# Kernel tuning notes

Hardware: AMD Instinct MI355X
Metric: run time of the kernel (lower is better)

Reference implementation:

```python
import jax, jax.numpy as jnp
import numpy as np

N, E, R, D = 50000, 640000, 200, 128  # nodes, edges, relations, feat dim (in_feat==out_feat)
EPS = 1e-5  # LayerNorm eps
NEG_SLOPE = 0.01  # F.leaky_relu default

def _xavier(k, shape):
    gain = np.sqrt(2.0)  # calculate_gain('relu')
    std = gain * np.sqrt(2.0 / (shape[0] + shape[1]))
    a = np.sqrt(3.0) * std
    return jax.random.uniform(k, shape, jnp.float32, -a, a)

def setup_inputs() -> dict:
    key = jax.random.key(0)
    ks = jax.random.split(key, 10)
    return {
        "node": jax.random.normal(ks[0], (N, D), jnp.float32),
        "rel": jax.random.normal(ks[1], (R, D), jnp.float32),
        "norm": jax.random.uniform(ks[2], (N, 1), jnp.float32),
        "w_triplet": _xavier(ks[3], (3 * D, D)),
        "w_quad": _xavier(ks[4], (D, D)),
        "loop_weight": _xavier(ks[5], (D, D)),
        "evolve_loop_weight": _xavier(ks[6], (D, D)),
        "src": jax.random.randint(ks[7], (E,), 0, N),
        "dst": jax.random.randint(ks[8], (E,), 0, N),
        "etype": jax.random.randint(ks[9], (E,), 0, R),
    }

def reference(node, rel, norm, w_triplet, w_quad, loop_weight, evolve_loop_weight, src, dst, etype):
    # triplet = cat([h_src, rel_emb, h_dst], 1) @ w_triplet, computed blockwise
    # to avoid materializing the [E, 3D] concat.
    W_s, W_r, W_d = w_triplet[:D], w_triplet[D:2 * D], w_triplet[2 * D:]
    triplet = node[src] @ W_s + rel[etype] @ W_r + node[dst] @ W_d  # [E, D]
    # 'fre' not in edata -> sro_fre is zeros; a_triplet = triplet @ w_quad
    a = jax.nn.leaky_relu(triplet @ w_quad, negative_slope=NEG_SLOPE)  # [E, D]
    # edge_softmax: softmax over incoming edges per destination node, per feature
    a_max = jax.ops.segment_max(a, dst, num_segments=N)
    a_max = jnp.where(jnp.isfinite(a_max), a_max, 0.0)  # empty segments -> -inf
    ex = jnp.exp(a - a_max[dst])
    denom = jax.ops.segment_sum(ex, dst, num_segments=N)
    att = ex / denom[dst]
    # weighted scatter-sum aggregation, then apply_func: h * norm
    h = jax.ops.segment_sum(att * triplet, dst, num_segments=N) * norm  # [N, D]
    # self-loop: evolve_loop_weight for in-degree-0 nodes, loop_weight otherwise
    indeg = jax.ops.segment_sum(jnp.ones((E,), jnp.float32), dst, num_segments=N)
    loop = jnp.where((indeg > 0)[:, None], node @ loop_weight, node @ evolve_loop_weight)
    out = h + loop
    # LayerNorm(elementwise_affine=False)
    mu = jnp.mean(out, axis=-1, keepdims=True)
    var = jnp.var(out, axis=-1, keepdims=True)
    return (out - mu) * jax.lax.rsqrt(var + EPS)
```

## Files before the change

### kernel.cpp

```cpp
#include <hip/hip_runtime.h>
#include <hip/hip_bf16.h>

#define D 128
#define LOG2E 1.4426950408889634f

typedef __attribute__((ext_vector_type(8))) short bf16x8;
typedef __attribute__((ext_vector_type(4))) float f32x4;

__device__ __forceinline__ unsigned short f2bf_bits(float f) {
    union { __hip_bfloat16 h; unsigned short u; } c;
    c.h = __float2bfloat16(f);
    return c.u;
}
__device__ __forceinline__ float bfbits2f(unsigned short u) {
    return __uint_as_float(((unsigned)u) << 16);
}
__device__ __forceinline__ float ldf(const void* p, size_t i, int f32) {
    return f32 ? ((const float*)p)[i] : bfbits2f(((const unsigned short*)p)[i]);
}
__device__ __forceinline__ void unpk(unsigned u, float& a, float& b) {
    a = __uint_as_float(u << 16);
    b = __uint_as_float(u & 0xFFFF0000u);
}

__global__ __launch_bounds__(256) void prep_kernel(
    const void* __restrict__ node, const void* __restrict__ wtrip,
    const void* __restrict__ wquad, const void* __restrict__ loopW,
    const void* __restrict__ evoW, unsigned short* __restrict__ wT,
    int* __restrict__ cnt, int* __restrict__ rank,
    const int* __restrict__ dst, int* __restrict__ flag, int E) {
    __shared__ int sflag;
    int tid = threadIdx.x;
    int bad = 0;
    if (tid < 64) {
        for (int j = 0; j < 4; j++) {
            float v = bfbits2f(((const unsigned short*)node)[tid + 64 * j]);
            if (!(fabsf(v) < 1e4f)) bad = 1;
        }
    }
    unsigned long long m = __ballot(bad);
    if (tid == 0) sflag = (m != 0ull) ? 1 : 0;
    __syncthreads();
    int f32 = sflag;
    int bx = blockIdx.x;
    if (bx == 0 && tid == 0) *flag = f32;

    if (bx < 192) {
        int unit = bx * 2 + (tid >> 7);
        int k = unit & 127, mjob = unit >> 7;
        int t = tid & 127;
        float acc = 0.f;
        for (int j = 0; j < D; j++)
            acc += ldf(wtrip, (size_t)mjob * D * D + (size_t)k * D + j, f32) *
                   ldf(wquad, (size_t)j * D + t, f32);
        const int jmap0 = (mjob == 0) ? 0 : (mjob == 1 ? 6 : 2);
        wT[(size_t)jmap0 * D * D + (size_t)t * D + k] = f2bf_bits(acc);
    } else if (bx < 272) {
        int u = bx - 192;
        int jr = u >> 4, seg = u & 15;
        const void* srcp; size_t base; int j;
        switch (jr) {
            case 0: srcp = wtrip; base = 0;             j = 1; break;
            case 1: srcp = wtrip; base = 2 * D * D;     j = 3; break;
            case 2: srcp = loopW; base = 0;             j = 4; break;
            case 3: srcp = evoW;  base = 0;             j = 5; break;
            default: srcp = wtrip; base = (size_t)D * D; j = 7; break;
        }
        for (int c = tid; c < 1024; c += 256) {
            int idx = seg * 1024 + c;
            int n = idx >> 7, k = idx & 127;
            unsigned short b = f32 ? f2bf_bits(((const float*)srcp)[base + (size_t)k * D + n])
                                   : ((const unsigned short*)srcp)[base + (size_t)k * D + n];
            wT[(size_t)j * D * D + (size_t)n * D + k] = b;
        }
    } else {
        int e = (bx - 272) * 256 + tid;
        if (e < E) rank[e] = atomicAdd(&cnt[dst[e]], 1);
    }
}

__global__ void scan_block(const int* __restrict__ cnt, int* __restrict__ offs,
                           int* __restrict__ part, int N) {
    __shared__ int sh[256];
    int tid = threadIdx.x;
    int i = blockIdx.x * 256 + tid;
    int v = (i < N) ? cnt[i] : 0;
    sh[tid] = v;
    __syncthreads();
    for (int o = 1; o < 256; o <<= 1) {
        int t = (tid >= o) ? sh[tid - o] : 0;
        __syncthreads();
        sh[tid] += t;
        __syncthreads();
    }
    if (i < N) offs[i] = sh[tid] - v;
    if (tid == 255) part[blockIdx.x] = sh[255];
}

__global__ void scan_fix(int* __restrict__ offs, const int* __restrict__ part,
                         int N, int E) {
    __shared__ int sh[256];
    int tid = threadIdx.x, b = blockIdx.x;
    sh[tid] = (tid < b) ? part[tid] : 0;
    __syncthreads();
    for (int o = 128; o; o >>= 1) {
        if (tid < o) sh[tid] += sh[tid + o];
        __syncthreads();
    }
    int carry = sh[0];
    int i = b * 256 + tid;
    if (i < N) offs[i] += carry;
    if (b == 0 && tid == 0) offs[N] = E;
}

__global__ __launch_bounds__(512) void gemm_kernel(
    const void* __restrict__ node, const void* __restrict__ rel,
    const unsigned short* __restrict__ wT, const int* __restrict__ cnt,
    unsigned* __restrict__ nodeST, unsigned* __restrict__ nodeDT,
    unsigned* __restrict__ relRT, unsigned* __restrict__ loopSel,
    const int* __restrict__ flag, int N, int R, int nodeBlocks,
    const int* __restrict__ src, const int* __restrict__ dst,
    const int* __restrict__ et, const int* __restrict__ offs,
    const int* __restrict__ rank, unsigned* __restrict__ ePack, int E) {
    __shared__ __align__(16) unsigned short Wt[D][D + 8];

    int bx = blockIdx.x, by = blockIdx.y;
    int tid = threadIdx.y * 64 + threadIdx.x;
    int isRel = 0, jp;
    if (bx >= nodeBlocks) {
        if (by == 1) {
            int e = (bx - nodeBlocks) * 512 + tid;
            if (e < E) {
                int d = dst[e];
                ePack[offs[d] + rank[e]] = (unsigned)src[e] | ((unsigned)et[e] << 20);
            }
            return;
        }
        if (by != 0 || bx - nodeBlocks >= (R + 127) / 128) return;
        isRel = 1;
        jp = 3;
    } else {
        jp = by;
    }

    int f32 = *flag;
    int rows = isRel ? R : N;
    int row0 = (isRel ? bx - nodeBlocks : bx) * 128;
    const void* A = isRel ? rel : node;

    int lane = threadIdx.x, wv = threadIdx.y;
    int l16 = lane & 15, quad = lane >> 4;
    int ar = row0 + wv * 16 + l16;
    int ar_c = ar < rows ? ar : rows - 1;

    int qIdx, tIdx;
    unsigned* O = nullptr;
    switch (jp) {
        case 0: qIdx = 0; tIdx = 1; O = nodeST; break;
        case 1: qIdx = 2; tIdx = 3; O = nodeDT; break;
        case 2: qIdx = 4; tIdx = 5; break;
        default: qIdx = 6; tIdx = 7; O = relRT; break;
    }

    bf16x8 af[4];
#pragma unroll
    for (int kk = 0; kk < 4; kk++) {
        int k = kk * 32 + quad * 8;
        if (f32) {
            const float* Af = (const float*)A + (size_t)ar_c * D + k;
#pragma unroll
            for (int j = 0; j < 8; j++) af[kk][j] = (short)f2bf_bits(Af[j]);
        } else {
            af[kk] = *(const bf16x8*)((const unsigned short*)A + (size_t)ar_c * D + k);
        }
    }

    const unsigned short* gQ = wT + (size_t)qIdx * D * D;
    const unsigned short* gT = wT + (size_t)tIdx * D * D;

    bf16x8 wreg[4], wreg2[4];
#pragma unroll
    for (int i = 0; i < 4; i++) {
        int c = tid + i * 512;
        wreg[i] = *(const bf16x8*)(gQ + (c >> 4) * 128 + (c & 15) * 8);
    }

    f32x4 accQ[8], accT[8];
#pragma unroll
    for (int i = 0; i < 8; i++) {
        accQ[i] = (f32x4){0.f, 0.f, 0.f, 0.f};
        accT[i] = (f32x4){0.f, 0.f, 0.f, 0.f};
    }

    for (int pass = 0; pass < 2; pass++) {
#pragma unroll
        for (int i = 0; i < 4; i++) {
            int c = tid + i * 512;
            *(bf16x8*)(&Wt[c >> 4][(c & 15) * 8]) = wreg[i];
        }
        if (pass == 0) {
#pragma unroll
            for (int i = 0; i < 4; i++) {
                int c = tid + i * 512;
                wreg2[i] = *(const bf16x8*)(gT + (c >> 4) * 128 + (c & 15) * 8);
            }
        }
        __syncthreads();
        f32x4* acc = pass ? accT : accQ;
#pragma unroll
        for (int kk = 0; kk < 4; kk++) {
#pragma unroll
            for (int nt = 0; nt < 8; nt++) {
                bf16x8 bfr = *(const bf16x8*)(&Wt[nt * 16 + l16][kk * 32 + quad * 8]);
                acc[nt] = __builtin_amdgcn_mfma_f32_16x16x32_bf16(af[kk], bfr, acc[nt], 0, 0, 0);
            }
        }
        __syncthreads();
#pragma unroll
        for (int i = 0; i < 4; i++) wreg[i] = wreg2[i];
    }

    int cr0 = row0 + wv * 16 + quad * 4;
    int odd = l16 & 1;
    if (jp != 2) {
#pragma unroll
        for (int r = 0; r < 4; r++) {
            int cr = cr0 + r;
#pragma unroll
            for (int nt = 0; nt < 8; nt++) {
                float vQ = accQ[nt][r] * LOG2E;
                float vT = accT[nt][r];
                float oQ = __shfl_xor(vQ, 1);
                float oT = __shfl_xor(vT, 1);
                unsigned w;
                if (!odd) w = (unsigned)f2bf_bits(vQ) | ((unsigned)f2bf_bits(oQ) << 16);
                else      w = (unsigned)f2bf_bits(oT) | ((unsigned)f2bf_bits(vT) << 16);
                if (cr < rows) O[(size_t)cr * 128 + nt * 16 + l16] = w;
            }
        }
    } else {
#pragma unroll
        for (int r = 0; r < 4; r++) {
            int cr = cr0 + r;
            int deg = (cr < rows) ? cnt[cr] : 0;
#pragma unroll
            for (int nt = 0; nt < 8; nt++) {
                float vL = accQ[nt][r], vE = accT[nt][r];
                float oL = __shfl_xor(vL, 1);
                float oE = __shfl_xor(vE, 1);
                unsigned wl, we;
                if (!odd) {
                    wl = (unsigned)f2bf_bits(vL) | ((unsigned)f2bf_bits(oL) << 16);
                    we = (unsigned)f2bf_bits(vE) | ((unsigned)f2bf_bits(oE) << 16);
                } else {
                    wl = (unsigned)f2bf_bits(oL) | ((unsigned)f2bf_bits(vL) << 16);
                    we = (unsigned)f2bf_bits(oE) | ((unsigned)f2bf_bits(vE) << 16);
                }
                if (cr < rows && !odd)
                    loopSel[(size_t)cr * 64 + nt * 8 + (l16 >> 1)] = (deg > 0) ? wl : we;
            }
        }
    }
}

__global__ __launch_bounds__(256) void agg_kernel(
    const int* __restrict__ offs, const unsigned* __restrict__ ePack,
    const uint2* __restrict__ ST, const uint2* __restrict__ RT,
    const uint2* __restrict__ DT, const unsigned* __restrict__ loopSel,
    const void* __restrict__ normv, void* __restrict__ out,
    const int* __restrict__ flag, int N) {
    int n = blockIdx.x * 4 + threadIdx.y;
    if (n >= N) return;
    int f32 = *flag;
    int lane = threadIdx.x;
    int start = offs[n], end = offs[n + 1];
    int deg = end - start;

    unsigned ul = loopSel[(size_t)n * 64 + lane];
    uint2 ud = DT[(size_t)n * 64 + lane];
    float qd0, qd1, td0, td1, acc0, acc1;
    unpk(ud.x, qd0, qd1);
    unpk(ud.y, td0, td1);
    unpk(ul, acc0, acc1);

    float den0 = 0.f, den1 = 0.f, h0 = 0.f, h1 = 0.f;
#define GATH(PK, US, UR)                                              \
    uint2 US = ST[(size_t)((PK) & 0xFFFFFu) * 64 + lane];             \
    uint2 UR = RT[(size_t)((PK) >> 20) * 64 + lane];
#define EMATH(US, UR)                                                 \
    {                                                                 \
        float qs0, qs1, qr0, qr1, ts0, ts1, tr0, tr1;                 \
        unpk(US.x, qs0, qs1); unpk(UR.x, qr0, qr1);                   \
        unpk(US.y, ts0, ts1); unpk(UR.y, tr0, tr1);                   \
        float q0 = qs0 + qr0 + qd0, q1 = qs1 + qr1 + qd1;             \
        float a0 = q0 > 0.f ? q0 : 0.01f * q0;                        \
        float a1 = q1 > 0.f ? q1 : 0.01f * q1;                        \
        float ex0 = exp2f(a0), ex1 = exp2f(a1);                       \
        den0 += ex0; den1 += ex1;                                     \
        h0 += ex0 * (ts0 + tr0 + td0);                                \
        h1 += ex1 * (ts1 + tr1 + td1);                                \
    }
    int e = start;
    for (; e + 3 < end; e += 4) {
        unsigned p0 = ePack[e], p1 = ePack[e + 1], p2 = ePack[e + 2], p3 = ePack[e + 3];
        GATH(p0, sA, rA)
        GATH(p1, sB, rB)
        GATH(p2, sC, rC)
        GATH(p3, sD, rD)
        EMATH(sA, rA)
        EMATH(sB, rB)
        EMATH(sC, rC)
        EMATH(sD, rD)
    }
    for (; e < end; e++) {
        unsigned pp = ePack[e];
        GATH(pp, sE, rE)
        EMATH(sE, rE)
    }

    float x0, x1;
    if (deg > 0) {
        float nrm = ldf(normv, n, f32);
        x0 = h0 / den0 * nrm + acc0;
        x1 = h1 / den1 * nrm + acc1;
    } else {
        x0 = acc0;
        x1 = acc1;
    }

    float s = x0 + x1, ss = x0 * x0 + x1 * x1;
#pragma unroll
    for (int o = 32; o; o >>= 1) {
        s += __shfl_xor(s, o);
        ss += __shfl_xor(ss, o);
    }
    float mu = s * (1.f / 128.f);
    float var = ss * (1.f / 128.f) - mu * mu;
    float rstd = rsqrtf(var + 1e-5f);
    float y0 = (x0 - mu) * rstd, y1 = (x1 - mu) * rstd;

    if (f32) {
        ((float2*)out)[(size_t)n * 64 + lane] = make_float2(y0, y1);
    } else {
        unsigned ob = (unsigned)f2bf_bits(y0) | ((unsigned)f2bf_bits(y1) << 16);
        ((unsigned*)out)[(size_t)n * 64 + lane] = ob;
    }
}

extern "C" void kernel_launch(void* const* d_in, const int* in_sizes, int n_in,
                              void* d_out, int out_size, void* d_ws, size_t ws_size,
                              hipStream_t stream) {
    const void* node = d_in[0];
    const void* rel = d_in[1];
    const void* normv = d_in[2];
    const void* wtrip = d_in[3];
    const void* wquad = d_in[4];
    const void* loopW = d_in[5];
    const void* evoW = d_in[6];
    const int* src = (const int*)d_in[7];
    const int* dst = (const int*)d_in[8];
    const int* et = (const int*)d_in[9];

    int N = in_sizes[0] / D;
    int R = in_sizes[1] / D;
    int E = in_sizes[7];
    int nb = (N + 255) / 256;
    int nodeBlocks = (N + 127) / 128;
    int relBlocks = (R + 127) / 128;
    int scatBlocks = (E + 511) / 512;

    char* p = (char*)d_ws;
    auto alloc = [&](size_t bytes) -> void* {
        void* r = (void*)p;
        p += (bytes + 255) & ~(size_t)255;
        return r;
    };
    unsigned* nodeST = (unsigned*)alloc((size_t)N * 128 * 4);
    unsigned* nodeDT = (unsigned*)alloc((size_t)N * 128 * 4);
    unsigned* relRT = (unsigned*)alloc((size_t)R * 128 * 4);
    unsigned* loopSel = (unsigned*)alloc((size_t)N * 64 * 4);
    unsigned short* wT = (unsigned short*)alloc((size_t)8 * D * D * 2);
    int* cnt = (int*)alloc((size_t)N * 4);
    int* offs = (int*)alloc((size_t)(N + 1) * 4);
    int* part = (int*)alloc((size_t)(nb + 1) * 4);
    int* rank = (int*)alloc((size_t)E * 4);
    unsigned* ePack = (unsigned*)alloc((size_t)E * 4);
    int* flag = (int*)alloc(4);

    hipMemsetAsync(cnt, 0, (size_t)N * 4, stream);
    prep_kernel<<<272 + (E + 255) / 256, 256, 0, stream>>>(
        node, wtrip, wquad, loopW, evoW, wT, cnt, rank, dst, flag, E);
    scan_block<<<nb, 256, 0, stream>>>(cnt, offs, part, N);
    scan_fix<<<nb, 256, 0, stream>>>(offs, part, N, E);
    int xext = nodeBlocks + (scatBlocks > relBlocks ? scatBlocks : relBlocks);
    gemm_kernel<<<dim3(xext, 3), dim3(64, 8), 0, stream>>>(
        node, rel, wT, cnt, nodeST, nodeDT, relRT, loopSel, flag, N, R, nodeBlocks,
        src, dst, et, offs, rank, ePack, E);
    agg_kernel<<<(N + 3) / 4, dim3(64, 4), 0, stream>>>(
        offs, ePack, (const uint2*)nodeST, (const uint2*)relRT, (const uint2*)nodeDT,
        loopSel, normv, d_out, flag, N);
}
```

Before: 235.2 us.

## Split wavefront into half-waves processing two edges at once with 16-byte gathers

The aggregation kernel now splits each 64-lane wavefront into two 32-lane halves. Each half handles a different edge, and each lane gathers 16 bytes (4 features of q and t) instead of 8. Partial softmax denominators and weighted sums are combined with a cross-half shuffle, the LayerNorm reduction runs over 32 lanes, and only the first half writes the output. The intent is to widen memory transactions and improve parallelism for low-degree nodes, at the cost of an extra shuffle and masked tail handling for odd degrees.

Result: no change. 236.9 us (+0.7%).

```diff
diff --git a/kernel.cpp b/kernel.cpp
--- a/kernel.cpp
+++ b/kernel.cpp
@@ -6,6 +6,9 @@
 
 typedef __attribute__((ext_vector_type(8))) short bf16x8;
 typedef __attribute__((ext_vector_type(4))) float f32x4;
+typedef __attribute__((ext_vector_type(2))) float f32x2;
+typedef __attribute__((ext_vector_type(2))) unsigned u32x2;
+typedef __attribute__((ext_vector_type(4))) unsigned u32x4;
 
 __device__ __forceinline__ unsigned short f2bf_bits(float f) {
     union { __hip_bfloat16 h; unsigned short u; } c;
@@ -18,9 +21,17 @@
 __device__ __forceinline__ float ldf(const void* p, size_t i, int f32) {
     return f32 ? ((const float*)p)[i] : bfbits2f(((const unsigned short*)p)[i]);
 }
-__device__ __forceinline__ void unpk(unsigned u, float& a, float& b) {
-    a = __uint_as_float(u << 16);
-    b = __uint_as_float(u & 0xFFFF0000u);
+__device__ __forceinline__ f32x2 unpk2(unsigned u) {
+    f32x2 r;
+    r.x = __uint_as_float(u << 16);
+    r.y = __uint_as_float(u & 0xFFFF0000u);
+    return r;
+}
+__device__ __forceinline__ f32x2 shx32(f32x2 v) {
+    f32x2 r;
+    r.x = __shfl_xor(v.x, 32);
+    r.y = __shfl_xor(v.y, 32);
+    return r;
 }
 
 __global__ __launch_bounds__(256) void prep_kernel(
@@ -265,85 +276,99 @@
 
 __global__ __launch_bounds__(256) void agg_kernel(
     const int* __restrict__ offs, const unsigned* __restrict__ ePack,
-    const uint2* __restrict__ ST, const uint2* __restrict__ RT,
-    const uint2* __restrict__ DT, const unsigned* __restrict__ loopSel,
+    const unsigned* __restrict__ ST, const unsigned* __restrict__ RT,
+    const unsigned* __restrict__ DT, const unsigned* __restrict__ loopSel,
     const void* __restrict__ normv, void* __restrict__ out,
     const int* __restrict__ flag, int N) {
     int n = blockIdx.x * 4 + threadIdx.y;
     if (n >= N) return;
     int f32 = *flag;
     int lane = threadIdx.x;
+    int half = lane >> 5, sl = lane & 31;
     int start = offs[n], end = offs[n + 1];
     int deg = end - start;
 
-    unsigned ul = loopSel[(size_t)n * 64 + lane];
-    uint2 ud = DT[(size_t)n * 64 + lane];
-    float qd0, qd1, td0, td1, acc0, acc1;
-    unpk(ud.x, qd0, qd1);
-    unpk(ud.y, td0, td1);
-    unpk(ul, acc0, acc1);
-
-    float den0 = 0.f, den1 = 0.f, h0 = 0.f, h1 = 0.f;
-#define GATH(PK, US, UR)                                              \
-    uint2 US = ST[(size_t)((PK) & 0xFFFFFu) * 64 + lane];             \
-    uint2 UR = RT[(size_t)((PK) >> 20) * 64 + lane];
-#define EMATH(US, UR)                                                 \
-    {                                                                 \
-        float qs0, qs1, qr0, qr1, ts0, ts1, tr0, tr1;                 \
-        unpk(US.x, qs0, qs1); unpk(UR.x, qr0, qr1);                   \
-        unpk(US.y, ts0, ts1); unpk(UR.y, tr0, tr1);                   \
-        float q0 = qs0 + qr0 + qd0, q1 = qs1 + qr1 + qd1;             \
-        float a0 = q0 > 0.f ? q0 : 0.01f * q0;                        \
-        float a1 = q1 > 0.f ? q1 : 0.01f * q1;                        \
-        float ex0 = exp2f(a0), ex1 = exp2f(a1);                       \
-        den0 += ex0; den1 += ex1;                                     \
-        h0 += ex0 * (ts0 + tr0 + td0);                                \
-        h1 += ex1 * (ts1 + tr1 + td1);                                \
-    }
+    u32x4 ud = *(const u32x4*)(DT + (size_t)n * 128 + sl * 4);
+    f32x2 qd01 = unpk2(ud.x), td01 = unpk2(ud.y);
+    f32x2 qd23 = unpk2(ud.z), td23 = unpk2(ud.w);
+    u32x2 ul = *(const u32x2*)(loopSel + (size_t)n * 64 + sl * 2);
+    f32x2 acc01 = unpk2(ul.x), acc23 = unpk2(ul.y);
+
+    const unsigned* STl = ST + sl * 4;
+    const unsigned* RTl = RT + sl * 4;
+
+    f32x2 den01 = {0.f, 0.f}, den23 = {0.f, 0.f};
+    f32x2 h01 = {0.f, 0.f}, h23 = {0.f, 0.f};
+
+#define PSTEP(PK, VM)                                                       \
+    {                                                                       \
+        unsigned pk_ = (PK);                                                \
+        u32x4 us = *(const u32x4*)(STl + (size_t)(pk_ & 0xFFFFFu) * 128);   \
+        u32x4 ur = *(const u32x4*)(RTl + (size_t)(pk_ >> 20) * 128);        \
+        f32x2 q01 = unpk2(us.x) + unpk2(ur.x) + qd01;                       \
+        f32x2 q23 = unpk2(us.z) + unpk2(ur.z) + qd23;                       \
+        f32x2 a01 = __builtin_elementwise_max(q01, q01 * 0.01f);            \
+        f32x2 a23 = __builtin_elementwise_max(q23, q23 * 0.01f);            \
+        f32x2 ex01, ex23;                                                   \
+        ex01.x = exp2f(a01.x); ex01.y = exp2f(a01.y);                       \
+        ex23.x = exp2f(a23.x); ex23.y = exp2f(a23.y);                       \
+        ex01 *= (VM); ex23 *= (VM);                                         \
+        den01 += ex01; den23 += ex23;                                       \
+        h01 += ex01 * (unpk2(us.y) + unpk2(ur.y) + td01);                   \
+        h23 += ex23 * (unpk2(us.w) + unpk2(ur.w) + td23);                   \
+    }
+
     int e = start;
     for (; e + 3 < end; e += 4) {
-        unsigned p0 = ePack[e], p1 = ePack[e + 1], p2 = ePack[e + 2], p3 = ePack[e + 3];
-        GATH(p0, sA, rA)
-        GATH(p1, sB, rB)
-        GATH(p2, sC, rC)
-        GATH(p3, sD, rD)
-        EMATH(sA, rA)
-        EMATH(sB, rB)
-        EMATH(sC, rC)
-        EMATH(sD, rD)
-    }
-    for (; e < end; e++) {
-        unsigned pp = ePack[e];
-        GATH(pp, sE, rE)
-        EMATH(sE, rE)
-    }
-
-    float x0, x1;
+        unsigned pA = ePack[e + half];
+        unsigned pB = ePack[e + 2 + half];
+        PSTEP(pA, 1.0f)
+        PSTEP(pB, 1.0f)
+    }
+    for (; e < end; e += 2) {
+        int eh = e + half;
+        int valid = eh < end;
+        unsigned pT = ePack[valid ? eh : end - 1];
+        PSTEP(pT, valid ? 1.0f : 0.0f)
+    }
+#undef PSTEP
+
+    den01 += shx32(den01); den23 += shx32(den23);
+    h01 += shx32(h01);     h23 += shx32(h23);
+
+    f32x2 x01, x23;
     if (deg > 0) {
         float nrm = ldf(normv, n, f32);
-        x0 = h0 / den0 * nrm + acc0;
-        x1 = h1 / den1 * nrm + acc1;
+        x01 = h01 / den01 * nrm + acc01;
+        x23 = h23 / den23 * nrm + acc23;
     } else {
-        x0 = acc0;
-        x1 = acc1;
-    }
-
-    float s = x0 + x1, ss = x0 * x0 + x1 * x1;
-#pragma unroll
-    for (int o = 32; o; o >>= 1) {
+        x01 = acc01;
+        x23 = acc23;
+    }
+
+    float s = (x01.x + x01.y) + (x23.x + x23.y);
+    float ss = (x01.x * x01.x + x01.y * x01.y) + (x23.x * x23.x + x23.y * x23.y);
+#pragma unroll
+    for (int o = 16; o; o >>= 1) {
         s += __shfl_xor(s, o);
         ss += __shfl_xor(ss, o);
     }
     float mu = s * (1.f / 128.f);
     float var = ss * (1.f / 128.f) - mu * mu;
     float rstd = rsqrtf(var + 1e-5f);
-    float y0 = (x0 - mu) * rstd, y1 = (x1 - mu) * rstd;
-
-    if (f32) {
-        ((float2*)out)[(size_t)n * 64 + lane] = make_float2(y0, y1);
-    } else {
-        unsigned ob = (unsigned)f2bf_bits(y0) | ((unsigned)f2bf_bits(y1) << 16);
-        ((unsigned*)out)[(size_t)n * 64 + lane] = ob;
+    f32x2 y01 = (x01 - mu) * rstd;
+    f32x2 y23 = (x23 - mu) * rstd;
+
+    if (half == 0) {
+        if (f32) {
+            float4 o4 = make_float4(y01.x, y01.y, y23.x, y23.y);
+            ((float4*)out)[(size_t)n * 32 + sl] = o4;
+        } else {
+            u32x2 ow;
+            ow.x = (unsigned)f2bf_bits(y01.x) | ((unsigned)f2bf_bits(y01.y) << 16);
+            ow.y = (unsigned)f2bf_bits(y23.x) | ((unsigned)f2bf_bits(y23.y) << 16);
+            *(u32x2*)((unsigned*)out + (size_t)n * 64 + sl * 2) = ow;
+        }
     }
 }
 
@@ -397,6 +422,5 @@
         node, rel, wT, cnt, nodeST, nodeDT, relRT, loopSel, flag, N, R, nodeBlocks,
         src, dst, et, offs, rank, ePack, E);
     agg_kernel<<<(N + 3) / 4, dim3(64, 4), 0, stream>>>(
-        offs, ePack, (const uint2*)nodeST, (const uint2*)relRT, (const uint2*)nodeDT,
-        loopSel, normv, d_out, flag, N);
-}
+        offs, ePack, nodeST, relRT, nodeDT, loopSel, normv, d_out, flag, N);
+}
```
